# Optimization experiments

Hardware: AMD Instinct MI355X
Metric: run time of the kernel (lower is better)

The kernel has to match this reference:

```python
import jax, jax.numpy as jnp
import numpy as np

N_NODES = 100000
N_EDGES = 1600000
IN_CH = 128
HID = 64
N_CLASSES = 16
N_GRAPHS = 64


def setup_inputs() -> dict:
    key = jax.random.key(0)
    ks = jax.random.split(key, 10)
    x = jax.random.normal(ks[0], (N_NODES, IN_CH), dtype=jnp.float32)
    edge_index = jax.random.randint(ks[1], (2, N_EDGES), 0, N_NODES, dtype=jnp.int64)
    edge_weight = jax.random.uniform(ks[2], (N_EDGES,), dtype=jnp.float32)
    batch = jnp.sort(jax.random.randint(ks[3], (N_NODES,), 0, N_GRAPHS, dtype=jnp.int64))
    s1 = 1.0 / np.sqrt(IN_CH)
    s2 = 1.0 / np.sqrt(HID)
    W1 = jax.random.uniform(ks[4], (IN_CH, HID), jnp.float32, -s1, s1)
    b1 = jnp.zeros((HID,), jnp.float32)
    W2 = jax.random.uniform(ks[5], (HID, HID), jnp.float32, -s2, s2)
    b2 = jnp.zeros((HID,), jnp.float32)
    Wl = jax.random.uniform(ks[6], (HID, N_CLASSES), jnp.float32, -s2, s2)
    bl = jax.random.uniform(ks[7], (N_CLASSES,), jnp.float32, -s2, s2)
    return {"x": x, "edge_index": edge_index, "edge_weight": edge_weight,
            "batch": batch, "W1": W1, "b1": b1, "W2": W2, "b2": b2,
            "Wl": Wl, "bl": bl}


def _gcn_conv(x, src, dst, ew, W, b, n_nodes):
    # PyG GCNConv: h = x @ W; symmetric normalization with self-loops;
    # out[dst] += norm * h[src]; out += bias.
    deg = jax.ops.segment_sum(ew, dst, num_segments=n_nodes)
    deg_inv_sqrt = jnp.where(deg > 0, jax.lax.rsqrt(jnp.maximum(deg, 1e-30)), 0.0)
    norm = deg_inv_sqrt[src] * ew * deg_inv_sqrt[dst]  # [E']
    h = x @ W                                          # [N, out]
    msg = h[src] * norm[:, None]                       # [E', out] gather
    out = jax.ops.segment_sum(msg, dst, num_segments=n_nodes)  # scatter-add
    return out + b


def reference(x, edge_index, edge_weight, batch, W1, b1, W2, b2, Wl, bl):
    n = x.shape[0]
    # add self loops once (weight 1.0), shared by both conv layers
    loop = jnp.arange(n, dtype=edge_index.dtype)
    src = jnp.concatenate([edge_index[0], loop])
    dst = jnp.concatenate([edge_index[1], loop])
    ew = jnp.concatenate([edge_weight, jnp.ones((n,), edge_weight.dtype)])

    h = jax.nn.relu(_gcn_conv(x, src, dst, ew, W1, b1, n))
    h = jax.nn.relu(_gcn_conv(h, src, dst, ew, W2, b2, n))

    # global_mean_pool over graphs
    sums = jax.ops.segment_sum(h, batch, num_segments=N_GRAPHS)  # [G, HID]
    cnt = jax.ops.segment_sum(jnp.ones((n,), h.dtype), batch, num_segments=N_GRAPHS)
    pooled = sums / jnp.maximum(cnt, 1.0)[:, None]

    return pooled @ Wl + bl
```

## Files before the change

kernel.cpp:

```cpp
#include <hip/hip_runtime.h>
#include <hip/hip_fp16.h>

#define N_NODES   100000
#define N_EDGES   1600000
#define IN_CH     128
#define HID       64
#define N_CLASSES 16
#define N_GRAPHS  64

#define BK_SH     9
#define BK_NODES  512
#define NB        ((N_NODES + BK_NODES - 1) / BK_NODES)
#define BK_CAP    10240
#define CH_EDGES  2048
#define EPT       8
#define NCH       ((N_EDGES + CH_EDGES - 1) / CH_EDGES)
#define AGG_NPW   8

typedef __attribute__((ext_vector_type(8))) short bf16x8;
typedef __attribute__((ext_vector_type(4))) float f32x4;

__device__ __forceinline__ unsigned short f2bf(float f) {
    unsigned u = __float_as_uint(f);
    u += 0x7fffu + ((u >> 16) & 1u);
    return (unsigned short)(u >> 16);
}
__device__ __forceinline__ float4 bf4(uint2 v) {
    float4 o;
    o.x = __uint_as_float(v.x << 16);
    o.y = __uint_as_float(v.x & 0xffff0000u);
    o.z = __uint_as_float(v.y << 16);
    o.w = __uint_as_float(v.y & 0xffff0000u);
    return o;
}
__device__ __forceinline__ float dec_ew(unsigned v) {
    return __half2float(__ushort_as_half((unsigned short)(v >> 17)));
}

__global__ void k_init(int* __restrict__ bcursor, float* __restrict__ pooled,
                       float* __restrict__ cnt) {
    int i = blockIdx.x * 256 + threadIdx.x;
    if (i < NB) bcursor[i] = i * BK_CAP;
    if (i < N_GRAPHS * HID) pooled[i] = 0.0f;
    if (i < N_GRAPHS) cnt[i] = 0.0f;
}

__global__ __launch_bounds__(256, 8) void k_binscatter(
        const int* __restrict__ src, const int* __restrict__ dst,
        const float* __restrict__ ew, int* __restrict__ bcursor,
        int2* __restrict__ bedges) {
    __shared__ int hist[NB];
    __shared__ int gbase[NB];
    const int t = threadIdx.x;
    const int base = blockIdx.x * CH_EDGES;

    for (int i = t; i < NB; i += 256) hist[i] = 0;
    __syncthreads();

    int myb[EPT], myr[EPT], myp[EPT]; float myw[EPT];
#pragma unroll
    for (int j = 0; j < EPT; ++j) {
        int i = base + j * 256 + t;
        if (i < N_EDGES) {
            int s = src[i], d = dst[i];
            int b = d >> BK_SH;
            myb[j] = b;
            myr[j] = atomicAdd(&hist[b], 1);
            myp[j] = s | ((d & (BK_NODES - 1)) << 17);
            myw[j] = ew[i];
        } else {
            myb[j] = -1;
        }
    }
    __syncthreads();

    if (t < NB) {
        int v = hist[t];
        gbase[t] = (v > 0) ? atomicAdd(&bcursor[t], v) : 0;
    }
    __syncthreads();

#pragma unroll
    for (int j = 0; j < EPT; ++j) {
        if (myb[j] >= 0)
            bedges[gbase[myb[j]] + myr[j]] =
                make_int2(myp[j], __float_as_int(myw[j]));
    }
}

__global__ __launch_bounds__(256) void k_build(const int* __restrict__ bcursor,
                                               const int2* __restrict__ bedges,
                                               int2* __restrict__ rowse,
                                               float* __restrict__ dis,
                                               unsigned* __restrict__ csr) {
    __shared__ int2  eds[BK_CAP];
    __shared__ int   cnt[BK_NODES];
    __shared__ float dsum[BK_NODES];
    __shared__ int   cur[BK_NODES];
    __shared__ int   sc[256];
    const int b = blockIdx.x;
    const int t = threadIdx.x;
    const int beg = b * BK_CAP, end = bcursor[b];
    const int n = end - beg;

    for (int i = t; i < BK_NODES; i += 256) { cnt[i] = 0; dsum[i] = 0.0f; }
    __syncthreads();

    for (int i = t; i < n; i += 256) {
        int2 e = bedges[beg + i];
        eds[i] = e;
        int dl = ((unsigned)e.x) >> 17;
        atomicAdd(&cnt[dl], 1);
        atomicAdd(&dsum[dl], __int_as_float(e.y));
    }
    __syncthreads();

    int a0 = cnt[2 * t], a1 = cnt[2 * t + 1];
    int pair = a0 + a1;
    sc[t] = pair;
    __syncthreads();
    for (int off = 1; off < 256; off <<= 1) {
        int a = (t >= off) ? sc[t - off] : 0;
        __syncthreads();
        sc[t] += a;
        __syncthreads();
    }
    int excl = sc[t] - pair;
    cur[2 * t] = excl;
    cur[2 * t + 1] = excl + a0;
    {
        int n0 = b * BK_NODES + 2 * t;
        if (n0 < N_NODES) {
            rowse[n0] = make_int2(beg + excl, beg + excl + a0);
            dis[n0] = rsqrtf(1.0f + dsum[2 * t]);
        }
        int n1 = n0 + 1;
        if (n1 < N_NODES) {
            rowse[n1] = make_int2(beg + excl + a0, beg + excl + a0 + a1);
            dis[n1] = rsqrtf(1.0f + dsum[2 * t + 1]);
        }
    }
    __syncthreads();

    for (int i = t; i < n; i += 256) {
        int2 e = eds[i];
        int dl = ((unsigned)e.x) >> 17;
        int s = e.x & 0x1FFFF;
        unsigned short w16 = __half_as_ushort(__float2half(__int_as_float(e.y)));
        int pos = beg + atomicAdd(&cur[dl], 1);
        csr[pos] = (unsigned)s | ((unsigned)w16 << 17);
    }
}

template <int K>
__global__ __launch_bounds__(256) void k_gemm(const float* __restrict__ x,
                                              const float* __restrict__ W,
                                              const float* __restrict__ dis,
                                              unsigned short* __restrict__ hb) {
    constexpr int AS = K + 8;
    __shared__ unsigned short a_s[64 * AS];
    __shared__ unsigned short wt[64 * AS];
    const int t    = threadIdx.x;
    const int lane = t & 63;
    const int wave = t >> 6;
    const int m    = lane & 15;
    const int quad = lane >> 4;
    const int rowbase = blockIdx.x * 64;

    constexpr int CPR = K / 8;
    for (int c = t; c < 64 * CPR; c += 256) {
        int row = c / CPR, cc = c % CPR;
        int gr = rowbase + row;
        float4 v0, v1;
        if (gr < N_NODES) {
            v0 = *(const float4*)&x[(long)gr * K + cc * 8];
            v1 = *(const float4*)&x[(long)gr * K + cc * 8 + 4];
        } else {
            v0 = make_float4(0.f, 0.f, 0.f, 0.f); v1 = v0;
        }
        uint4 p;
        p.x = f2bf(v0.x) | ((unsigned)f2bf(v0.y) << 16);
        p.y = f2bf(v0.z) | ((unsigned)f2bf(v0.w) << 16);
        p.z = f2bf(v1.x) | ((unsigned)f2bf(v1.y) << 16);
        p.w = f2bf(v1.z) | ((unsigned)f2bf(v1.w) << 16);
        *(uint4*)&a_s[row * AS + cc * 8] = p;
    }
    for (int idx = t; idx < K * 64; idx += 256) {
        int k = idx >> 6, n = idx & 63;
        wt[n * AS + k] = f2bf(W[idx]);
    }
    __syncthreads();

    bf16x8 bfrag[4][K / 32];
#pragma unroll
    for (int nt = 0; nt < 4; ++nt)
#pragma unroll
        for (int ks = 0; ks < K / 32; ++ks)
            bfrag[nt][ks] = *(const bf16x8*)&wt[(nt * 16 + m) * AS + ks * 32 + quad * 8];

    f32x4 acc[4];
#pragma unroll
    for (int nt = 0; nt < 4; ++nt) acc[nt] = (f32x4){0.f, 0.f, 0.f, 0.f};

#pragma unroll
    for (int ks = 0; ks < K / 32; ++ks) {
        bf16x8 af = *(const bf16x8*)&a_s[(wave * 16 + m) * AS + ks * 32 + quad * 8];
#pragma unroll
        for (int nt = 0; nt < 4; ++nt)
            acc[nt] = __builtin_amdgcn_mfma_f32_16x16x32_bf16(af, bfrag[nt][ks],
                                                              acc[nt], 0, 0, 0);
    }

#pragma unroll
    for (int i = 0; i < 4; ++i) {
        int gr = rowbase + wave * 16 + quad * 4 + i;
        if (gr < N_NODES) {
            float dsc = dis[gr];
#pragma unroll
            for (int nt = 0; nt < 4; ++nt)
                hb[(long)gr * HID + nt * 16 + m] = f2bf(dsc * acc[nt][i]);
        }
    }
}

__global__ __launch_bounds__(256) void k_gemm2(const unsigned short* __restrict__ xb,
                                               const float* __restrict__ W,
                                               const float* __restrict__ dis,
                                               unsigned short* __restrict__ hb) {
    constexpr int K = HID;
    constexpr int AS = K + 8;
    __shared__ unsigned short a_s[64 * AS];
    __shared__ unsigned short wt[64 * AS];
    const int t    = threadIdx.x;
    const int lane = t & 63;
    const int wave = t >> 6;
    const int m    = lane & 15;
    const int quad = lane >> 4;
    const int rowbase = blockIdx.x * 64;

    for (int c = t; c < 64 * 8; c += 256) {
        int row = c >> 3, cc = c & 7;
        int gr = rowbase + row;
        uint4 p = (gr < N_NODES) ? *(const uint4*)&xb[(long)gr * K + cc * 8]
                                 : make_uint4(0, 0, 0, 0);
        *(uint4*)&a_s[row * AS + cc * 8] = p;
    }
    for (int idx = t; idx < K * 64; idx += 256) {
        int k = idx >> 6, n = idx & 63;
        wt[n * AS + k] = f2bf(W[idx]);
    }
    __syncthreads();

    bf16x8 bfrag[4][K / 32];
#pragma unroll
    for (int nt = 0; nt < 4; ++nt)
#pragma unroll
        for (int ks = 0; ks < K / 32; ++ks)
            bfrag[nt][ks] = *(const bf16x8*)&wt[(nt * 16 + m) * AS + ks * 32 + quad * 8];

    f32x4 acc[4];
#pragma unroll
    for (int nt = 0; nt < 4; ++nt) acc[nt] = (f32x4){0.f, 0.f, 0.f, 0.f};

#pragma unroll
    for (int ks = 0; ks < K / 32; ++ks) {
        bf16x8 af = *(const bf16x8*)&a_s[(wave * 16 + m) * AS + ks * 32 + quad * 8];
#pragma unroll
        for (int nt = 0; nt < 4; ++nt)
            acc[nt] = __builtin_amdgcn_mfma_f32_16x16x32_bf16(af, bfrag[nt][ks],
                                                              acc[nt], 0, 0, 0);
    }

#pragma unroll
    for (int i = 0; i < 4; ++i) {
        int gr = rowbase + wave * 16 + quad * 4 + i;
        if (gr < N_NODES) {
            float dsc = dis[gr];
#pragma unroll
            for (int nt = 0; nt < 4; ++nt)
                hb[(long)gr * HID + nt * 16 + m] = f2bf(dsc * acc[nt][i]);
        }
    }
}

template <bool OUT_BF16>
__global__ void k_aggregate(const int2* __restrict__ rowse, const unsigned* __restrict__ csr,
                            const uint2* __restrict__ hb, const float* __restrict__ dis,
                            const float* __restrict__ b, float4* __restrict__ out4,
                            ushort4* __restrict__ outb) {
    const int tid  = threadIdx.x;
    const int lane = tid & 63;
    const int g    = lane >> 4;
    const int c4   = lane & 15;
    const int nodebase = (blockIdx.x * 4 + (tid >> 6)) * AGG_NPW;
    const float4 bb = ((const float4*)b)[c4];

    if (nodebase >= N_NODES) return;

    int2 rs = rowse[nodebase];
    uint2 hsr = hb[nodebase * 16 + c4];

    for (int j = 0; j < AGG_NPW; ++j) {
        const int node = nodebase + j;
        if (node >= N_NODES) return;

        const int2 rs_c = rs;
        const float4 hs = bf4(hsr);
        if (j + 1 < AGG_NPW && node + 1 < N_NODES) {
            rs  = rowse[node + 1];
            hsr = hb[(node + 1) * 16 + c4];
        }

        float4 acc;
        if (g == 0) { acc = hs; }
        else        { acc.x = 0.f; acc.y = 0.f; acc.z = 0.f; acc.w = 0.f; }

        int p = rs_c.x;
        const int end = rs_c.y;

        unsigned d0, d1, d2, d3;
        if (p + 16 <= end) {
            d0 = csr[p + g];     d1 = csr[p + 4 + g];
            d2 = csr[p + 8 + g]; d3 = csr[p + 12 + g];
        }
        while (p + 16 <= end) {
            const unsigned e0 = d0, e1 = d1, e2 = d2, e3 = d3;
            const int pn = p + 16;
            if (pn + 16 <= end) {
                d0 = csr[pn + g];     d1 = csr[pn + 4 + g];
                d2 = csr[pn + 8 + g]; d3 = csr[pn + 12 + g];
            }
            float4 v0 = bf4(hb[(e0 & 0x1FFFF) * 16 + c4]);
            float4 v1 = bf4(hb[(e1 & 0x1FFFF) * 16 + c4]);
            float4 v2 = bf4(hb[(e2 & 0x1FFFF) * 16 + c4]);
            float4 v3 = bf4(hb[(e3 & 0x1FFFF) * 16 + c4]);
            float w0 = dec_ew(e0), w1 = dec_ew(e1);
            float w2 = dec_ew(e2), w3 = dec_ew(e3);
            acc.x += w0 * v0.x; acc.y += w0 * v0.y; acc.z += w0 * v0.z; acc.w += w0 * v0.w;
            acc.x += w1 * v1.x; acc.y += w1 * v1.y; acc.z += w1 * v1.z; acc.w += w1 * v1.w;
            acc.x += w2 * v2.x; acc.y += w2 * v2.y; acc.z += w2 * v2.z; acc.w += w2 * v2.w;
            acc.x += w3 * v3.x; acc.y += w3 * v3.y; acc.z += w3 * v3.z; acc.w += w3 * v3.w;
            p = pn;
        }
        if (p < end) {
            int i0 = p + g, i1 = p + 4 + g, i2 = p + 8 + g, i3 = p + 12 + g;
            unsigned e0 = csr[min(i0, end - 1)];
            unsigned e1 = csr[min(i1, end - 1)];
            unsigned e2 = csr[min(i2, end - 1)];
            unsigned e3 = csr[min(i3, end - 1)];
            float4 v0 = bf4(hb[(e0 & 0x1FFFF) * 16 + c4]);
            float4 v1 = bf4(hb[(e1 & 0x1FFFF) * 16 + c4]);
            float4 v2 = bf4(hb[(e2 & 0x1FFFF) * 16 + c4]);
            float4 v3 = bf4(hb[(e3 & 0x1FFFF) * 16 + c4]);
            float w0 = (i0 < end) ? dec_ew(e0) : 0.0f;
            float w1 = (i1 < end) ? dec_ew(e1) : 0.0f;
            float w2 = (i2 < end) ? dec_ew(e2) : 0.0f;
            float w3 = (i3 < end) ? dec_ew(e3) : 0.0f;
            acc.x += w0 * v0.x; acc.y += w0 * v0.y; acc.z += w0 * v0.z; acc.w += w0 * v0.w;
            acc.x += w1 * v1.x; acc.y += w1 * v1.y; acc.z += w1 * v1.z; acc.w += w1 * v1.w;
            acc.x += w2 * v2.x; acc.y += w2 * v2.y; acc.z += w2 * v2.z; acc.w += w2 * v2.w;
            acc.x += w3 * v3.x; acc.y += w3 * v3.y; acc.z += w3 * v3.z; acc.w += w3 * v3.w;
        }

        acc.x += __shfl_xor(acc.x, 16); acc.y += __shfl_xor(acc.y, 16);
        acc.z += __shfl_xor(acc.z, 16); acc.w += __shfl_xor(acc.w, 16);
        acc.x += __shfl_xor(acc.x, 32); acc.y += __shfl_xor(acc.y, 32);
        acc.z += __shfl_xor(acc.z, 32); acc.w += __shfl_xor(acc.w, 32);

        if (g == 0) {
            const float dd = dis[node];
            float4 o;
            o.x = fmaxf(dd * acc.x + bb.x, 0.0f);
            o.y = fmaxf(dd * acc.y + bb.y, 0.0f);
            o.z = fmaxf(dd * acc.z + bb.z, 0.0f);
            o.w = fmaxf(dd * acc.w + bb.w, 0.0f);
            if (OUT_BF16) {
                ushort4 ob;
                ob.x = f2bf(o.x); ob.y = f2bf(o.y);
                ob.z = f2bf(o.z); ob.w = f2bf(o.w);
                outb[node * 16 + c4] = ob;
            } else {
                out4[node * 16 + c4] = o;
            }
        }
    }
}

#define POOL_NPB 256
__global__ __launch_bounds__(1024) void k_pool(const float* __restrict__ agg,
                                               const int* __restrict__ batch,
                                               float* __restrict__ pooled,
                                               float* __restrict__ cnt) {
    __shared__ float psh[N_GRAPHS * HID];
    __shared__ float csh[N_GRAPHS];
    const int tid = threadIdx.x;
    const int c = tid & 63;
    const int w = tid >> 6;
    const int nodebase = blockIdx.x * POOL_NPB + w * 16;

    for (int i = tid; i < N_GRAPHS * HID; i += 1024) psh[i] = 0.f;
    if (tid < N_GRAPHS) csh[tid] = 0.f;
    __syncthreads();

    int curg = -1; float accv = 0.f, cntacc = 0.f;
    for (int j = 0; j < 16; ++j) {
        int node = nodebase + j;
        if (node >= N_NODES) break;
        int g = batch[node];
        float v = agg[node * HID + c];
        if (g != curg) {
            if (curg >= 0) {
                atomicAdd(&psh[curg * HID + c], accv);
                if (c == 0) atomicAdd(&csh[curg], cntacc);
            }
            curg = g; accv = 0.f; cntacc = 0.f;
        }
        accv += v; cntacc += 1.f;
    }
    if (curg >= 0) {
        atomicAdd(&psh[curg * HID + c], accv);
        if (c == 0) atomicAdd(&csh[curg], cntacc);
    }
    __syncthreads();

    for (int i = tid; i < N_GRAPHS * HID; i += 1024) {
        if (csh[i >> 6] > 0.f) atomicAdd(&pooled[i], psh[i]);
    }
    if (tid < N_GRAPHS && csh[tid] > 0.f) atomicAdd(&cnt[tid], csh[tid]);
}

__global__ void k_out(const float* __restrict__ pooled, const float* __restrict__ cnt,
                      const float* __restrict__ Wl, const float* __restrict__ bl,
                      float* __restrict__ out) {
    int tid = threadIdx.x;
    int g = tid >> 4, k = tid & 15;
    float inv = 1.0f / fmaxf(cnt[g], 1.0f);
    float acc = 0.f;
#pragma unroll
    for (int h = 0; h < HID; ++h) acc += pooled[g * HID + h] * Wl[h * N_CLASSES + k];
    out[g * N_CLASSES + k] = acc * inv + bl[k];
}

extern "C" void kernel_launch(void* const* d_in, const int* in_sizes, int n_in,
                              void* d_out, int out_size, void* d_ws, size_t ws_size,
                              hipStream_t stream) {
    const float* x     = (const float*)d_in[0];
    const int*   ei    = (const int*)d_in[1];
    const float* ew    = (const float*)d_in[2];
    const int*   batch = (const int*)d_in[3];
    const float* W1    = (const float*)d_in[4];
    const float* b1    = (const float*)d_in[5];
    const float* W2    = (const float*)d_in[6];
    const float* b2    = (const float*)d_in[7];
    const float* Wl    = (const float*)d_in[8];
    const float* bl    = (const float*)d_in[9];

    const int* srcv = ei;
    const int* dstv = ei + N_EDGES;

    char* wsb = (char*)d_ws;
    float*          dis    = (float*)wsb;              wsb += 100352 * 4;
    int2*           rowse  = (int2*)wsb;               wsb += 100352 * 8;
    int*            bcursor= (int*)wsb;                wsb += 256 * 4;
    unsigned*       csr    = (unsigned*)wsb;           wsb += (size_t)NB * BK_CAP * 4;
    unsigned short* hb     = (unsigned short*)wsb;     wsb += N_NODES * HID * 2;
    unsigned short* hbn    = (unsigned short*)wsb;     wsb += N_NODES * HID * 2;
    float*          agg    = (float*)wsb;              wsb += N_NODES * HID * 4;
    float*          pooled = (float*)wsb;              wsb += N_GRAPHS * HID * 4;
    float*          cnt    = (float*)wsb;              wsb += N_GRAPHS * 4;
    float*          out    = (float*)d_out;
    int2*           bedges = (int2*)agg;

    k_init<<<16, 256, 0, stream>>>(bcursor, pooled, cnt);
    k_binscatter<<<NCH, 256, 0, stream>>>(srcv, dstv, ew, bcursor, bedges);
    k_build<<<NB, 256, 0, stream>>>(bcursor, bedges, rowse, dis, csr);

    const int agg_blocks = (N_NODES + 4 * AGG_NPW - 1) / (4 * AGG_NPW);

    k_gemm<IN_CH><<<(N_NODES + 63) / 64, 256, 0, stream>>>(x, W1, dis, hb);
    k_aggregate<true><<<agg_blocks, 256, 0, stream>>>(rowse, csr, (const uint2*)hb,
                                                      dis, b1, nullptr, (ushort4*)hbn);
    k_gemm2<<<(N_NODES + 63) / 64, 256, 0, stream>>>(hbn, W2, dis, hb);
    k_aggregate<false><<<agg_blocks, 256, 0, stream>>>(rowse, csr, (const uint2*)hb,
                                                       dis, b2, (float4*)agg, nullptr);

    k_pool<<<(N_NODES + POOL_NPB - 1) / POOL_NPB, 1024, 0, stream>>>(
        agg, batch, pooled, cnt);
    k_out<<<1, N_GRAPHS * N_CLASSES, 0, stream>>>(pooled, cnt, Wl, bl, out);
}
```

Measured before the change: 281.1 us.

## Stage binned edges in shared memory for coalesced scatter writes

```diff
diff --git a/kernel.cpp b/kernel.cpp
--- a/kernel.cpp
+++ b/kernel.cpp
@@ -12,8 +12,8 @@
 #define BK_NODES  512
 #define NB        ((N_NODES + BK_NODES - 1) / BK_NODES)
 #define BK_CAP    10240
-#define CH_EDGES  2048
-#define EPT       8
+#define CH_EDGES  4096
+#define EPT       16
 #define NCH       ((N_EDGES + CH_EDGES - 1) / CH_EDGES)
 #define AGG_NPW   8
 
@@ -45,14 +45,18 @@
     if (i < N_GRAPHS) cnt[i] = 0.0f;
 }
 
-__global__ __launch_bounds__(256, 8) void k_binscatter(
-        const int* __restrict__ src, const int* __restrict__ dst,
-        const float* __restrict__ ew, int* __restrict__ bcursor,
-        int2* __restrict__ bedges) {
-    __shared__ int hist[NB];
-    __shared__ int gbase[NB];
+__global__ void k_binscatter(const int* __restrict__ src, const int* __restrict__ dst,
+                             const float* __restrict__ ew, int* __restrict__ bcursor,
+                             int2* __restrict__ bedges) {
+    __shared__ int  hist[NB];
+    __shared__ int  offs[NB];
+    __shared__ int  gbase[NB];
+    __shared__ int  sc[256];
+    __shared__ int2 stage[CH_EDGES];
+    __shared__ int  dest[CH_EDGES];
     const int t = threadIdx.x;
     const int base = blockIdx.x * CH_EDGES;
+    const int nloc = min(CH_EDGES, N_EDGES - base);
 
     for (int i = t; i < NB; i += 256) hist[i] = 0;
     __syncthreads();
@@ -74,18 +78,33 @@
     }
     __syncthreads();
 
+    int v = (t < NB) ? hist[t] : 0;
+    sc[t] = v;
+    __syncthreads();
+    for (int off = 1; off < 256; off <<= 1) {
+        int a = (t >= off) ? sc[t - off] : 0;
+        __syncthreads();
+        sc[t] += a;
+        __syncthreads();
+    }
     if (t < NB) {
-        int v = hist[t];
+        offs[t] = sc[t] - v;
         gbase[t] = (v > 0) ? atomicAdd(&bcursor[t], v) : 0;
     }
     __syncthreads();
 
 #pragma unroll
     for (int j = 0; j < EPT; ++j) {
-        if (myb[j] >= 0)
-            bedges[gbase[myb[j]] + myr[j]] =
-                make_int2(myp[j], __float_as_int(myw[j]));
-    }
+        if (myb[j] >= 0) {
+            int p = offs[myb[j]] + myr[j];
+            stage[p] = make_int2(myp[j], __float_as_int(myw[j]));
+            dest[p] = gbase[myb[j]] + myr[j];
+        }
+    }
+    __syncthreads();
+
+    for (int i = t; i < nloc; i += 256)
+        bedges[dest[i]] = stage[i];
 }
 
 __global__ __launch_bounds__(256) void k_build(const int* __restrict__ bcursor,
```

New measurement: 275.2 us. -2.1%, faster.
